# Performance work log

Hardware: AMD Instinct MI355X
Metric: run time of the kernel (lower is better)

Reference implementation:

```python
import jax, jax.numpy as jnp
import numpy as np

N, E_RAW, F_IN, H, C = 50000, 800000, 500, 5, 32
HID = H * C  # 160
NEG_GAT = 0.2   # GATConv leaky_relu slope for attention logits
NEG = 0.01      # F.leaky_relu default slope
LN_EPS = 1e-5


def glorot(key, shape):
    fan_in, fan_out = shape[0], shape[-1]
    lim = jnp.sqrt(6.0 / (fan_in + fan_out))
    return jax.random.uniform(key, shape, jnp.float32, -lim, lim)


def setup_inputs() -> dict:
    key = jax.random.key(0)
    ks = jax.random.split(key, 12)
    x = jax.random.normal(ks[0], (N, F_IN), jnp.float32)
    edge_index = jax.random.randint(ks[1], (2, E_RAW), 0, N, jnp.int64)
    return {
        "x": x,
        "edge_index": edge_index,
        "W1": glorot(ks[2], (F_IN, HID)),
        "att1_s": glorot(ks[3], (H, C)),
        "att1_d": glorot(ks[4], (H, C)),
        "b1": jnp.zeros((HID,), jnp.float32),
        "g1": jnp.ones((HID,), jnp.float32),
        "be1": jnp.zeros((HID,), jnp.float32),
        "W2": glorot(ks[5], (HID, HID)),
        "att2_s": glorot(ks[6], (H, C)),
        "att2_d": glorot(ks[7], (H, C)),
        "b2": jnp.zeros((HID,), jnp.float32),
        "Wm": glorot(ks[8], (HID, HID)),
        "bm": jnp.zeros((HID,), jnp.float32),
    }


def add_self_loops(edge_index):
    loops = jnp.arange(N, dtype=edge_index.dtype)
    return jnp.concatenate([edge_index, jnp.stack([loops, loops])], axis=1)


def gat_conv(x, src, dst, W, att_s, att_d, bias):
    # x: [N, Fin] -> per-head transform [N, H, C]
    xl = (x @ W).reshape(N, H, C)
    a_s = jnp.einsum('nhc,hc->nh', xl, att_s)  # [N, H]
    a_d = jnp.einsum('nhc,hc->nh', xl, att_d)
    logits = jax.nn.leaky_relu(a_s[src] + a_d[dst], NEG_GAT)  # [E, H]
    # segment softmax over incoming edges of each dst node
    lmax = jax.ops.segment_max(logits, dst, num_segments=N)
    alpha = jnp.exp(logits - lmax[dst])
    denom = jax.ops.segment_sum(alpha, dst, num_segments=N)
    alpha = alpha / (denom[dst] + 1e-16)
    msg = xl[src] * alpha[:, :, None]  # [E, H, C]
    out = jax.ops.segment_sum(msg, dst, num_segments=N)
    return out.reshape(N, HID) + bias, alpha


def layer_norm(x, g, b):
    mu = jnp.mean(x, axis=-1, keepdims=True)
    var = jnp.mean((x - mu) ** 2, axis=-1, keepdims=True)
    return (x - mu) * jax.lax.rsqrt(var + LN_EPS) * g + b


def reference(x, edge_index, W1, att1_s, att1_d, b1, g1, be1,
              W2, att2_s, att2_d, b2, Wm, bm):
    ei = add_self_loops(edge_index)
    src, dst = ei[0], ei[1]
    h, alpha1 = gat_conv(x, src, dst, W1, att1_s, att1_d, b1)
    h = jax.nn.leaky_relu(h, NEG)
    h = layer_norm(h, g1, be1)  # dropout is identity in eval mode
    h, alpha2 = gat_conv(h, src, dst, W2, att2_s, att2_d, b2)
    h = jax.nn.leaky_relu(h, NEG)
    out = jax.nn.leaky_relu(h @ Wm + bm, NEG)
    return out, alpha1, alpha2
```

## Files before the change

kernel.cpp:

```cpp
#include <hip/hip_runtime.h>

#define N_NODES 50000
#define E_RAW_N 800000
#define E_TOT   850000
#define F_IN_K  500
#define HID     160
#define XSTR    192

using short8 = __attribute__((ext_vector_type(8))) short;
using f32x4  = __attribute__((ext_vector_type(4))) float;

__device__ __forceinline__ float b2f(unsigned short u) {
  union { unsigned int i; float f; } v; v.i = ((unsigned int)u) << 16; return v.f;
}
__device__ __forceinline__ unsigned short f2b(float f) {
  union { float f; unsigned int i; } v; v.f = f;
  unsigned int i = v.i;
  unsigned int lsb = (i >> 16) & 1u;
  i += 0x7fffu + lsb;
  return (unsigned short)(i >> 16);
}

__device__ __forceinline__ float wsum(float x) {
  #pragma unroll
  for (int o = 32; o; o >>= 1) x += __shfl_xor(x, o, 64);
  return x;
}
__device__ __forceinline__ float wmax(float x) {
  #pragma unroll
  for (int o = 32; o; o >>= 1) x = fmaxf(x, __shfl_xor(x, o, 64));
  return x;
}
__device__ __forceinline__ float lrelu2(float x) { return x > 0.f ? x : 0.2f * x; }

__global__ void detect_kernel(const int* __restrict__ ei, int* __restrict__ flag) {
  if (threadIdx.x == 0 && blockIdx.x == 0) {
    int allz = 1;
    for (int i = 1; i < 128; i += 2) if (ei[i] != 0) { allz = 0; break; }
    *flag = allz;
  }
}
__device__ __forceinline__ int edge_src(const int* ei, int wide, int e) {
  return wide ? ei[2 * e] : ei[e];
}
__device__ __forceinline__ int edge_dst(const int* ei, int wide, int e) {
  return wide ? ei[2 * (E_RAW_N + e)] : ei[E_RAW_N + e];
}

__global__ __launch_bounds__(256) void convert_all(
    const float* __restrict__ W1, const float* __restrict__ W2, const float* __restrict__ Wm,
    unsigned short* __restrict__ Bt1, unsigned short* __restrict__ Bt2,
    unsigned short* __restrict__ Btm)
{
  const int i = blockIdx.x * 256 + threadIdx.x;
  if (i < HID * 512) {
    const int c = i / 512, k = i % 512;
    Bt1[i] = f2b((k < F_IN_K) ? W1[(long)k * HID + c] : 0.f);
  }
  if (i < HID * 192) {
    const int c = i / 192, k = i % 192;
    Bt2[i] = f2b((k < HID) ? W2[(long)k * HID + c] : 0.f);
    Btm[i] = f2b((k < HID) ? Wm[(long)k * HID + c] : 0.f);
  }
}

template<typename AT, int K, int KPAD, int BK, int MODE>
__global__ __launch_bounds__(128) void gemm_lds(
    const AT* __restrict__ A, const unsigned short* __restrict__ Bt,
    float* __restrict__ C, unsigned short* __restrict__ Ch,
    const float* __restrict__ bias,
    const float* __restrict__ att_s, const float* __restrict__ att_d,
    float* __restrict__ a_d)
{
  constexpr bool AB16 = (sizeof(AT) == 2);
  constexpr int LSTR = BK + 8;
  constexpr int CHUNKS = KPAD / BK;
  constexpr int KSC = BK / 32;
  constexpr int ROWU = BK / 8;
  constexpr int UNITS = HID * ROWU;
  static_assert(UNITS % 128 == 0, "units must tile threads");
  constexpr int UPT = UNITS / 128;
  __shared__ __align__(16) unsigned short Bs[HID][LSTR];

  const int t = threadIdx.x;
  const int l = t & 63;
  const int w = t >> 6;
  const int m = l & 15;
  const int kgrp = (l >> 4) * 8;
  const int rbase = blockIdx.x * 32 + w * 16;
  const int arow = (rbase + m < N_NODES) ? rbase + m : N_NODES - 1;
  const AT* Arow = A + (long)arow * K;

  f32x4 acc[10];
  #pragma unroll
  for (int i = 0; i < 10; ++i) acc[i] = (f32x4){0.f, 0.f, 0.f, 0.f};

  short8 rb[UPT];
  float  arF[KSC][8], arF2[KSC][8];
  short8 arS[KSC], arS2[KSC];

  auto loadB = [&](int cc, short8* dst) {
    #pragma unroll
    for (int i = 0; i < UPT; ++i) {
      const int u = i * 128 + t;
      const int c = u / ROWU;
      const int k8 = u % ROWU;
      dst[i] = *(const short8*)(Bt + (long)c * KPAD + cc * BK + k8 * 8);
    }
  };
  auto loadA = [&](int cc, float aF[KSC][8], short8* aS) {
    #pragma unroll
    for (int ks = 0; ks < KSC; ++ks) {
      const int kb = cc * BK + ks * 32 + kgrp;
      if constexpr (AB16) {
        short8 v = (short8){0,0,0,0,0,0,0,0};
        if (kb + 8 <= K) v = *(const short8*)(Arow + kb);
        else if (kb < K) {
          #pragma unroll
          for (int j = 0; j < 8; ++j) v[j] = (kb + j < K) ? (short)Arow[kb + j] : (short)0;
        }
        aS[ks] = v;
      } else {
        if (kb + 8 <= K) {
          const float4 a0 = *(const float4*)(Arow + kb);
          const float4 a1 = *(const float4*)(Arow + kb + 4);
          aF[ks][0]=a0.x; aF[ks][1]=a0.y; aF[ks][2]=a0.z; aF[ks][3]=a0.w;
          aF[ks][4]=a1.x; aF[ks][5]=a1.y; aF[ks][6]=a1.z; aF[ks][7]=a1.w;
        } else {
          #pragma unroll
          for (int j = 0; j < 8; ++j) aF[ks][j] = (kb + j < K) ? (float)Arow[kb + j] : 0.f;
        }
      }
    }
  };

  loadB(0, rb);
  loadA(0, arF, arS);

  for (int cc = 0; cc < CHUNKS; ++cc) {
    __syncthreads();
    #pragma unroll
    for (int i = 0; i < UPT; ++i) {
      const int u = i * 128 + t;
      const int c = u / ROWU;
      const int k8 = u % ROWU;
      *(short8*)&Bs[c][k8 * 8] = rb[i];
    }
    __syncthreads();
    if (cc + 1 < CHUNKS) {
      loadB(cc + 1, rb);
      loadA(cc + 1, arF2, arS2);
      __builtin_amdgcn_sched_barrier(0);
    }
    __builtin_amdgcn_s_setprio(1);
    #pragma unroll
    for (int ks = 0; ks < KSC; ++ks) {
      short8 ah;
      if constexpr (AB16) {
        ah = arS[ks];
      } else {
        #pragma unroll
        for (int j = 0; j < 8; ++j) ah[j] = (short)f2b(arF[ks][j]);
      }
      #pragma unroll
      for (int ct = 0; ct < 10; ++ct) {
        const short8 bh = *(const short8*)&Bs[ct * 16 + m][ks * 32 + kgrp];
        acc[ct] = __builtin_amdgcn_mfma_f32_16x16x32_bf16(ah, bh, acc[ct], 0, 0, 0);
      }
    }
    __builtin_amdgcn_s_setprio(0);
    if (cc + 1 < CHUNKS) {
      #pragma unroll
      for (int ks = 0; ks < KSC; ++ks) {
        if constexpr (AB16) arS[ks] = arS2[ks];
        else {
          #pragma unroll
          for (int j = 0; j < 8; ++j) arF[ks][j] = arF2[ks][j];
        }
      }
    }
  }

  const int crow0 = rbase + (l >> 4) * 4;

  if (MODE == 2) {
    #pragma unroll
    for (int r = 0; r < 4; ++r) {
      float ps[5], pd[5];
      #pragma unroll
      for (int h = 0; h < 5; ++h) {
        float s = acc[2*h][r]     * att_s[(2*h) * 16 + m]
                + acc[2*h + 1][r] * att_s[(2*h + 1) * 16 + m];
        float d = acc[2*h][r]     * att_d[(2*h) * 16 + m]
                + acc[2*h + 1][r] * att_d[(2*h + 1) * 16 + m];
        #pragma unroll
        for (int o = 1; o < 16; o <<= 1) {
          s += __shfl_xor(s, o, 64);
          d += __shfl_xor(d, o, 64);
        }
        ps[h] = s; pd[h] = d;
      }
      const int crow = crow0 + r;
      if (crow < N_NODES && m < 5) {
        const float vs = m == 0 ? ps[0] : m == 1 ? ps[1] : m == 2 ? ps[2] : m == 3 ? ps[3] : ps[4];
        const float vd = m == 0 ? pd[0] : m == 1 ? pd[1] : m == 2 ? pd[2] : m == 3 ? pd[3] : pd[4];
        ((float*)(Ch + (long)crow * XSTR + 160))[m] = vs;
        a_d[crow * 5 + m] = vd;
      }
    }
  }

  #pragma unroll
  for (int r = 0; r < 4; ++r) {
    const int crow = crow0 + r;
    if (crow < N_NODES) {
      #pragma unroll
      for (int ct = 0; ct < 10; ++ct) {
        const int col = ct * 16 + m;
        float v = acc[ct][r];
        if (MODE == 1) { v += bias[col]; v = v > 0.f ? v : 0.01f * v; }
        if (MODE == 2) Ch[(long)crow * XSTR + col] = f2b(v);
        else           C[(long)crow * HID + col] = v;
      }
    }
  }
}

__global__ __launch_bounds__(256) void count_kernel(const int* __restrict__ ei,
    const int* __restrict__ flag, int* __restrict__ deg) {
  const int e = blockIdx.x * 256 + threadIdx.x;
  if (e >= E_TOT) return;
  const int wide = *flag;
  const int d = (e < E_RAW_N) ? edge_dst(ei, wide, e) : (e - E_RAW_N);
  atomicAdd(&deg[d], 1);
}

#define SCAN_CHUNK 49
__global__ __launch_bounds__(1024) void scan_kernel(const int* __restrict__ deg, int* __restrict__ off) {
  __shared__ int wtot[16];
  const int t = threadIdx.x;
  const int lane = t & 63, wid = t >> 6;
  const int base = t * SCAN_CHUNK;
  int local[SCAN_CHUNK];
  int sum = 0;
  #pragma unroll
  for (int i = 0; i < SCAN_CHUNK; ++i) {
    const int idx = base + i;
    const int v = (idx < N_NODES) ? deg[idx] : 0;
    local[i] = sum;
    sum += v;
  }
  int inc = sum;
  #pragma unroll
  for (int o = 1; o < 64; o <<= 1) {
    const int y = __shfl_up(inc, o, 64);
    if (lane >= o) inc += y;
  }
  if (lane == 63) wtot[wid] = inc;
  __syncthreads();
  if (wid == 0 && lane < 16) {
    const int v = wtot[lane];
    int inc2 = v;
    #pragma unroll
    for (int o = 1; o < 16; o <<= 1) {
      const int y = __shfl_up(inc2, o, 64);
      if (lane >= o) inc2 += y;
    }
    wtot[lane] = inc2 - v;
  }
  __syncthreads();
  const int pre = wtot[wid] + (inc - sum);
  #pragma unroll
  for (int i = 0; i < SCAN_CHUNK; ++i) {
    const int idx = base + i;
    if (idx < N_NODES) off[idx] = pre + local[i];
  }
  if (t == 1023) off[N_NODES] = E_TOT;
}

__global__ __launch_bounds__(256) void fill_kernel(const int* __restrict__ ei,
    const int* __restrict__ flag, const int* __restrict__ off,
    int* __restrict__ fillc, int* __restrict__ csr_src, int* __restrict__ csr_eid) {
  const int e = blockIdx.x * 256 + threadIdx.x;
  if (e >= E_TOT) return;
  const int wide = *flag;
  int s, d;
  if (e < E_RAW_N) { s = edge_src(ei, wide, e); d = edge_dst(ei, wide, e); }
  else { s = e - E_RAW_N; d = s; }
  const int p = off[d] + atomicAdd(&fillc[d], 1);
  csr_src[p] = s;
  csr_eid[p] = e;
}

template<int DO_LN>
__global__ __launch_bounds__(256) void node_kernel(
    const int* __restrict__ off_, const int* __restrict__ csr_src, const int* __restrict__ csr_eid,
    const unsigned short* __restrict__ xlh,
    const float* __restrict__ a_d,
    float* __restrict__ alpha_out,
    const float* __restrict__ bias,
    const float* __restrict__ gamma_, const float* __restrict__ beta_,
    unsigned short* __restrict__ hout)
{
  __shared__ int   srcS[4][64];
  __shared__ float alS[4][64][6];

  const int w = threadIdx.x >> 6;
  const int l = threadIdx.x & 63;
  const int n = blockIdx.x * 4 + w;
  if (n >= N_NODES) return;
  const int off = off_[n];
  const int deg = off_[n + 1] - off;

  const float ad0 = a_d[n*5+0], ad1 = a_d[n*5+1], ad2 = a_d[n*5+2], ad3 = a_d[n*5+3], ad4 = a_d[n*5+4];
  const int hA = l >> 4;
  float accx = 0.f, accy = 0.f, accz = 0.f;

  if (deg <= 64) {
    int src = 0, eid = 0;
    float e0 = 0.f, e1 = 0.f, e2 = 0.f, e3 = 0.f, e4 = 0.f;
    if (l < deg) {
      src = csr_src[off + l];
      eid = csr_eid[off + l];
      const float* ap = (const float*)(xlh + (unsigned)src * XSTR + 160);
      e0 = __expf(lrelu2(ap[0] + ad0));
      e1 = __expf(lrelu2(ap[1] + ad1));
      e2 = __expf(lrelu2(ap[2] + ad2));
      e3 = __expf(lrelu2(ap[3] + ad3));
      e4 = __expf(lrelu2(ap[4] + ad4));
    }
    const float i0 = 1.f / (wsum(e0) + 1e-16f), i1 = 1.f / (wsum(e1) + 1e-16f),
                i2 = 1.f / (wsum(e2) + 1e-16f), i3 = 1.f / (wsum(e3) + 1e-16f),
                i4 = 1.f / (wsum(e4) + 1e-16f);
    const float a0 = e0 * i0, a1 = e1 * i1, a2 = e2 * i2, a3 = e3 * i3, a4 = e4 * i4;
    if (l < deg) {
      float* aw = alpha_out + (long)eid * 5;
      aw[0] = a0; aw[1] = a1; aw[2] = a2; aw[3] = a3; aw[4] = a4;
    }
    srcS[w][l] = src;
    alS[w][l][0] = a0; alS[w][l][1] = a1; alS[w][l][2] = a2;
    alS[w][l][3] = a3; alS[w][l][4] = a4;

    const int degR = (deg + 7) & ~7;
    const unsigned cx = 2 * l, cz = 128 + l;
    for (int s0 = 0; s0 < degR; s0 += 8) {
      int sr[8]; float aA[8], aB[8];
      #pragma unroll
      for (int j = 0; j < 8; ++j) {
        sr[j] = srcS[w][s0 + j];
        aA[j] = alS[w][s0 + j][hA];
        aB[j] = alS[w][s0 + j][4];
      }
      ushort2 u2[8]; unsigned short z[8];
      #pragma unroll
      for (int j = 0; j < 8; ++j) {
        const unsigned xb = (unsigned)sr[j] * XSTR;
        u2[j] = *(const ushort2*)(xlh + xb + cx);
        if (l < 32) z[j] = xlh[xb + cz];
      }
      #pragma unroll
      for (int j = 0; j < 8; ++j) {
        accx += b2f(u2[j].x) * aA[j];
        accy += b2f(u2[j].y) * aA[j];
        if (l < 32) accz += b2f(z[j]) * aB[j];
      }
    }
  } else {
    float m0 = -1e30f, m1 = -1e30f, m2 = -1e30f, m3 = -1e30f, m4 = -1e30f;
    for (int s = l; s < deg; s += 64) {
      const float* ap = (const float*)(xlh + (unsigned)csr_src[off + s] * XSTR + 160);
      m0 = fmaxf(m0, lrelu2(ap[0] + ad0));
      m1 = fmaxf(m1, lrelu2(ap[1] + ad1));
      m2 = fmaxf(m2, lrelu2(ap[2] + ad2));
      m3 = fmaxf(m3, lrelu2(ap[3] + ad3));
      m4 = fmaxf(m4, lrelu2(ap[4] + ad4));
    }
    m0 = wmax(m0); m1 = wmax(m1); m2 = wmax(m2); m3 = wmax(m3); m4 = wmax(m4);
    float s0 = 0.f, s1 = 0.f, s2 = 0.f, s3 = 0.f, s4 = 0.f;
    for (int s = l; s < deg; s += 64) {
      const float* ap = (const float*)(xlh + (unsigned)csr_src[off + s] * XSTR + 160);
      s0 += __expf(lrelu2(ap[0] + ad0) - m0);
      s1 += __expf(lrelu2(ap[1] + ad1) - m1);
      s2 += __expf(lrelu2(ap[2] + ad2) - m2);
      s3 += __expf(lrelu2(ap[3] + ad3) - m3);
      s4 += __expf(lrelu2(ap[4] + ad4) - m4);
    }
    const float i0 = 1.f / (wsum(s0) + 1e-16f), i1 = 1.f / (wsum(s1) + 1e-16f),
                i2 = 1.f / (wsum(s2) + 1e-16f), i3 = 1.f / (wsum(s3) + 1e-16f),
                i4 = 1.f / (wsum(s4) + 1e-16f);
    const float adA = hA == 0 ? ad0 : hA == 1 ? ad1 : hA == 2 ? ad2 : ad3;
    const float mA  = hA == 0 ? m0  : hA == 1 ? m1  : hA == 2 ? m2  : m3;
    const float iA  = hA == 0 ? i0  : hA == 1 ? i1  : hA == 2 ? i2  : i3;
    float adw = 0.f, mw = 0.f, iw = 0.f;
    if (l < 5) {
      adw = l == 0 ? ad0 : l == 1 ? ad1 : l == 2 ? ad2 : l == 3 ? ad3 : ad4;
      mw  = l == 0 ? m0  : l == 1 ? m1  : l == 2 ? m2  : l == 3 ? m3  : m4;
      iw  = l == 0 ? i0  : l == 1 ? i1  : l == 2 ? i2  : l == 3 ? i3  : i4;
    }
    for (int s = 0; s < deg; ++s) {
      const int p = off + s;
      const int srcs = csr_src[p];
      const unsigned xb = (unsigned)srcs * XSTR;
      const float* ap = (const float*)(xlh + xb + 160);
      const float aA = __expf(lrelu2(ap[hA] + adA) - mA) * iA;
      const ushort2 u2 = *(const ushort2*)(xlh + xb + 2 * l);
      accx += b2f(u2.x) * aA;
      accy += b2f(u2.y) * aA;
      if (l < 32) {
        const float aC = __expf(lrelu2(ap[4] + ad4) - m4) * i4;
        accz += b2f(xlh[xb + 128 + l]) * aC;
      }
      if (l < 5) {
        alpha_out[(long)csr_eid[p] * 5 + l] = __expf(lrelu2(ap[l] + adw) - mw) * iw;
      }
    }
  }

  const int c0 = 2 * l, c2 = 128 + l;
  float v0 = accx + bias[c0];     v0 = v0 > 0.f ? v0 : 0.01f * v0;
  float v1 = accy + bias[c0 + 1]; v1 = v1 > 0.f ? v1 : 0.01f * v1;
  float v2 = 0.f;
  if (l < 32) { v2 = accz + bias[c2]; v2 = v2 > 0.f ? v2 : 0.01f * v2; }

  const long hb = (long)n * HID;
  if (DO_LN) {
    const float tot = wsum(v0 + v1 + v2);
    const float mean = tot * (1.f / 160.f);
    const float d0 = v0 - mean, d1 = v1 - mean;
    float sq = d0 * d0 + d1 * d1;
    float d2 = 0.f;
    if (l < 32) { d2 = v2 - mean; sq += d2 * d2; }
    const float var = wsum(sq) * (1.f / 160.f);
    const float rstd = rsqrtf(var + 1e-5f);
    hout[hb + c0]     = f2b(d0 * rstd * gamma_[c0]     + beta_[c0]);
    hout[hb + c0 + 1] = f2b(d1 * rstd * gamma_[c0 + 1] + beta_[c0 + 1]);
    if (l < 32) hout[hb + c2] = f2b(d2 * rstd * gamma_[c2] + beta_[c2]);
  } else {
    hout[hb + c0]     = f2b(v0);
    hout[hb + c0 + 1] = f2b(v1);
    if (l < 32) hout[hb + c2] = f2b(v2);
  }
}

extern "C" void kernel_launch(void* const* d_in, const int* in_sizes, int n_in,
                              void* d_out, int out_size, void* d_ws, size_t ws_size,
                              hipStream_t stream)
{
  const float* x     = (const float*)d_in[0];
  const int*   ei    = (const int*)d_in[1];
  const float* W1    = (const float*)d_in[2];
  const float* att1s = (const float*)d_in[3];
  const float* att1d = (const float*)d_in[4];
  const float* b1    = (const float*)d_in[5];
  const float* g1    = (const float*)d_in[6];
  const float* be1   = (const float*)d_in[7];
  const float* W2    = (const float*)d_in[8];
  const float* att2s = (const float*)d_in[9];
  const float* att2d = (const float*)d_in[10];
  const float* b2    = (const float*)d_in[11];
  const float* Wm    = (const float*)d_in[12];
  const float* bm    = (const float*)d_in[13];

  float* out    = (float*)d_out;
  float* alpha1 = out + (long)N_NODES * HID;
  float* alpha2 = alpha1 + (long)E_TOT * 5;

  char* p = (char*)d_ws;
  auto alloc = [&](size_t bytes) { void* r = (void*)p; p += (bytes + 255) & ~(size_t)255; return r; };
  unsigned short* hb16 = (unsigned short*)alloc((size_t)N_NODES * HID * 2);
  unsigned short* xlh  = (unsigned short*)alloc((size_t)N_NODES * XSTR * 2);
  float* ad_  = (float*)alloc((size_t)N_NODES * 5 * 4);
  int* deg    = (int*)alloc((size_t)N_NODES * 4);
  int* fillc  = (int*)alloc((size_t)N_NODES * 4);
  int* off    = (int*)alloc((size_t)(N_NODES + 1) * 4);
  int* csrS   = (int*)alloc((size_t)E_TOT * 4);
  int* csrE   = (int*)alloc((size_t)E_TOT * 4);
  int* flag   = (int*)alloc(256);
  unsigned short* Bt1 = (unsigned short*)alloc((size_t)HID * 512 * 2);
  unsigned short* Bt2 = (unsigned short*)alloc((size_t)HID * 192 * 2);
  unsigned short* Btm = (unsigned short*)alloc((size_t)HID * 192 * 2);

  hipMemsetAsync(deg, 0, (size_t)N_NODES * 4, stream);
  hipMemsetAsync(fillc, 0, (size_t)N_NODES * 4, stream);

  detect_kernel<<<1, 64, 0, stream>>>(ei, flag);
  const int EB = (E_TOT + 255) / 256;
  count_kernel<<<EB, 256, 0, stream>>>(ei, flag, deg);
  scan_kernel<<<1, 1024, 0, stream>>>(deg, off);
  fill_kernel<<<EB, 256, 0, stream>>>(ei, flag, off, fillc, csrS, csrE);

  convert_all<<<(HID * 512 + 255) / 256, 256, 0, stream>>>(W1, W2, Wm, Bt1, Bt2, Btm);

  const int GB = (N_NODES + 31) / 32;

  gemm_lds<float, F_IN_K, 512, 64, 2><<<GB, 128, 0, stream>>>(x, Bt1, nullptr, xlh, nullptr, att1s, att1d, ad_);
  node_kernel<1><<<N_NODES / 4, 256, 0, stream>>>(off, csrS, csrE, xlh, ad_, alpha1, b1, g1, be1, hb16);

  gemm_lds<unsigned short, HID, 192, 64, 2><<<GB, 128, 0, stream>>>(hb16, Bt2, nullptr, xlh, nullptr, att2s, att2d, ad_);
  node_kernel<0><<<N_NODES / 4, 256, 0, stream>>>(off, csrS, csrE, xlh, ad_, alpha2, b2, nullptr, nullptr, hb16);

  gemm_lds<unsigned short, HID, 192, 64, 1><<<GB, 128, 0, stream>>>(hb16, Btm, out, nullptr, bm, nullptr, nullptr, nullptr);
}
```

Before: 399.5 us.

## Stream GEMM B tiles directly into swizzled double-buffered LDS via global_load_lds

Pre-swizzles the bf16 weight matrices into 32-wide K chunks with an XOR pattern. The GEMM now copies each chunk straight from global memory into one of two LDS buffers using global_load_lds, so B no longer passes through registers. This also removes one barrier per chunk and shrinks the K step from 64 to 32, which lowers register pressure but doubles the number of loop iterations. The two degree/fill memsets are merged into one contiguous memset.

```diff
diff --git a/kernel.cpp b/kernel.cpp
--- a/kernel.cpp
+++ b/kernel.cpp
@@ -6,6 +6,7 @@
 #define F_IN_K  500
 #define HID     160
 #define XSTR    192
+#define CHELEMS (HID * 32)
 
 using short8 = __attribute__((ext_vector_type(8))) short;
 using f32x4  = __attribute__((ext_vector_type(4))) float;
@@ -32,6 +33,16 @@
   return x;
 }
 __device__ __forceinline__ float lrelu2(float x) { return x > 0.f ? x : 0.2f * x; }
+
+__device__ __forceinline__ void gload16(const unsigned short* g, unsigned short* l) {
+  __builtin_amdgcn_global_load_lds(
+      (const __attribute__((address_space(1))) void*)g,
+      (__attribute__((address_space(3))) void*)l, 16, 0, 0);
+}
+
+__device__ __forceinline__ int bswz(int c, int kk) {
+  return ((c << 5) | kk) ^ ((c & 7) << 3);
+}
 
 __global__ void detect_kernel(const int* __restrict__ ei, int* __restrict__ flag) {
   if (threadIdx.x == 0 && blockIdx.x == 0) {
@@ -55,16 +66,18 @@
   const int i = blockIdx.x * 256 + threadIdx.x;
   if (i < HID * 512) {
     const int c = i / 512, k = i % 512;
-    Bt1[i] = f2b((k < F_IN_K) ? W1[(long)k * HID + c] : 0.f);
+    const int idx = (k >> 5) * CHELEMS + bswz(c, k & 31);
+    Bt1[idx] = f2b((k < F_IN_K) ? W1[(long)k * HID + c] : 0.f);
   }
   if (i < HID * 192) {
     const int c = i / 192, k = i % 192;
-    Bt2[i] = f2b((k < HID) ? W2[(long)k * HID + c] : 0.f);
-    Btm[i] = f2b((k < HID) ? Wm[(long)k * HID + c] : 0.f);
-  }
-}
-
-template<typename AT, int K, int KPAD, int BK, int MODE>
+    const int idx = (k >> 5) * CHELEMS + bswz(c, k & 31);
+    Bt2[idx] = f2b((k < HID) ? W2[(long)k * HID + c] : 0.f);
+    Btm[idx] = f2b((k < HID) ? Wm[(long)k * HID + c] : 0.f);
+  }
+}
+
+template<typename AT, int K, int KPAD, int MODE>
 __global__ __launch_bounds__(128) void gemm_lds(
     const AT* __restrict__ A, const unsigned short* __restrict__ Bt,
     float* __restrict__ C, unsigned short* __restrict__ Ch,
@@ -73,14 +86,8 @@
     float* __restrict__ a_d)
 {
   constexpr bool AB16 = (sizeof(AT) == 2);
-  constexpr int LSTR = BK + 8;
-  constexpr int CHUNKS = KPAD / BK;
-  constexpr int KSC = BK / 32;
-  constexpr int ROWU = BK / 8;
-  constexpr int UNITS = HID * ROWU;
-  static_assert(UNITS % 128 == 0, "units must tile threads");
-  constexpr int UPT = UNITS / 128;
-  __shared__ __align__(16) unsigned short Bs[HID][LSTR];
+  constexpr int CHUNKS = KPAD / 32;
+  __shared__ __align__(16) unsigned short Bs[2][CHELEMS];
 
   const int t = threadIdx.x;
   const int l = t & 63;
@@ -95,88 +102,71 @@
   #pragma unroll
   for (int i = 0; i < 10; ++i) acc[i] = (f32x4){0.f, 0.f, 0.f, 0.f};
 
-  short8 rb[UPT];
-  float  arF[KSC][8], arF2[KSC][8];
-  short8 arS[KSC], arS2[KSC];
-
-  auto loadB = [&](int cc, short8* dst) {
+  float  arF[8], arF2[8];
+  short8 arS, arS2;
+
+  auto issueB = [&](int cc) {
+    const unsigned short* src = Bt + (long)cc * CHELEMS;
+    unsigned short* dst = &Bs[cc & 1][0];
     #pragma unroll
-    for (int i = 0; i < UPT; ++i) {
-      const int u = i * 128 + t;
-      const int c = u / ROWU;
-      const int k8 = u % ROWU;
-      dst[i] = *(const short8*)(Bt + (long)c * KPAD + cc * BK + k8 * 8);
+    for (int j = 0; j < 5; ++j) {
+      const int base = (j * 2 + w) * 512;
+      gload16(src + base + l * 8, dst + base);
     }
   };
-  auto loadA = [&](int cc, float aF[KSC][8], short8* aS) {
-    #pragma unroll
-    for (int ks = 0; ks < KSC; ++ks) {
-      const int kb = cc * BK + ks * 32 + kgrp;
-      if constexpr (AB16) {
-        short8 v = (short8){0,0,0,0,0,0,0,0};
-        if (kb + 8 <= K) v = *(const short8*)(Arow + kb);
-        else if (kb < K) {
-          #pragma unroll
-          for (int j = 0; j < 8; ++j) v[j] = (kb + j < K) ? (short)Arow[kb + j] : (short)0;
-        }
-        aS[ks] = v;
+  auto loadA = [&](int cc, float* aF, short8& aS) {
+    const int kb = cc * 32 + kgrp;
+    if constexpr (AB16) {
+      short8 v = (short8){0,0,0,0,0,0,0,0};
+      if (kb + 8 <= K) v = *(const short8*)(Arow + kb);
+      else if (kb < K) {
+        #pragma unroll
+        for (int j = 0; j < 8; ++j) v[j] = (kb + j < K) ? (short)Arow[kb + j] : (short)0;
+      }
+      aS = v;
+    } else {
+      if (kb + 8 <= K) {
+        const float4 a0 = *(const float4*)(Arow + kb);
+        const float4 a1 = *(const float4*)(Arow + kb + 4);
+        aF[0]=a0.x; aF[1]=a0.y; aF[2]=a0.z; aF[3]=a0.w;
+        aF[4]=a1.x; aF[5]=a1.y; aF[6]=a1.z; aF[7]=a1.w;
       } else {
-        if (kb + 8 <= K) {
-          const float4 a0 = *(const float4*)(Arow + kb);
-          const float4 a1 = *(const float4*)(Arow + kb + 4);
-          aF[ks][0]=a0.x; aF[ks][1]=a0.y; aF[ks][2]=a0.z; aF[ks][3]=a0.w;
-          aF[ks][4]=a1.x; aF[ks][5]=a1.y; aF[ks][6]=a1.z; aF[ks][7]=a1.w;
-        } else {
-          #pragma unroll
-          for (int j = 0; j < 8; ++j) aF[ks][j] = (kb + j < K) ? (float)Arow[kb + j] : 0.f;
-        }
+        #pragma unroll
+        for (int j = 0; j < 8; ++j) aF[j] = (kb + j < K) ? (float)Arow[kb + j] : 0.f;
       }
     }
   };
 
-  loadB(0, rb);
+  issueB(0);
   loadA(0, arF, arS);
 
   for (int cc = 0; cc < CHUNKS; ++cc) {
     __syncthreads();
-    #pragma unroll
-    for (int i = 0; i < UPT; ++i) {
-      const int u = i * 128 + t;
-      const int c = u / ROWU;
-      const int k8 = u % ROWU;
-      *(short8*)&Bs[c][k8 * 8] = rb[i];
-    }
-    __syncthreads();
     if (cc + 1 < CHUNKS) {
-      loadB(cc + 1, rb);
+      issueB(cc + 1);
       loadA(cc + 1, arF2, arS2);
       __builtin_amdgcn_sched_barrier(0);
     }
     __builtin_amdgcn_s_setprio(1);
+    short8 ah;
+    if constexpr (AB16) {
+      ah = arS;
+    } else {
+      #pragma unroll
+      for (int j = 0; j < 8; ++j) ah[j] = (short)f2b(arF[j]);
+    }
     #pragma unroll
-    for (int ks = 0; ks < KSC; ++ks) {
-      short8 ah;
-      if constexpr (AB16) {
-        ah = arS[ks];
-      } else {
-        #pragma unroll
-        for (int j = 0; j < 8; ++j) ah[j] = (short)f2b(arF[ks][j]);
-      }
-      #pragma unroll
-      for (int ct = 0; ct < 10; ++ct) {
-        const short8 bh = *(const short8*)&Bs[ct * 16 + m][ks * 32 + kgrp];
-        acc[ct] = __builtin_amdgcn_mfma_f32_16x16x32_bf16(ah, bh, acc[ct], 0, 0, 0);
-      }
+    for (int ct = 0; ct < 10; ++ct) {
+      const int c = ct * 16 + m;
+      const short8 bh = *(const short8*)&Bs[cc & 1][bswz(c, kgrp)];
+      acc[ct] = __builtin_amdgcn_mfma_f32_16x16x32_bf16(ah, bh, acc[ct], 0, 0, 0);
     }
     __builtin_amdgcn_s_setprio(0);
     if (cc + 1 < CHUNKS) {
-      #pragma unroll
-      for (int ks = 0; ks < KSC; ++ks) {
-        if constexpr (AB16) arS[ks] = arS2[ks];
-        else {
-          #pragma unroll
-          for (int j = 0; j < 8; ++j) arF[ks][j] = arF2[ks][j];
-        }
+      if constexpr (AB16) arS = arS2;
+      else {
+        #pragma unroll
+        for (int j = 0; j < 8; ++j) arF[j] = arF2[j];
       }
     }
   }
@@ -480,8 +470,7 @@
   unsigned short* Bt2 = (unsigned short*)alloc((size_t)HID * 192 * 2);
   unsigned short* Btm = (unsigned short*)alloc((size_t)HID * 192 * 2);
 
-  hipMemsetAsync(deg, 0, (size_t)N_NODES * 4, stream);
-  hipMemsetAsync(fillc, 0, (size_t)N_NODES * 4, stream);
+  hipMemsetAsync(deg, 0, (size_t)((char*)off - (char*)deg), stream);
 
   detect_kernel<<<1, 64, 0, stream>>>(ei, flag);
   const int EB = (E_TOT + 255) / 256;
@@ -493,11 +482,11 @@
 
   const int GB = (N_NODES + 31) / 32;
 
-  gemm_lds<float, F_IN_K, 512, 64, 2><<<GB, 128, 0, stream>>>(x, Bt1, nullptr, xlh, nullptr, att1s, att1d, ad_);
+  gemm_lds<float, F_IN_K, 512, 2><<<GB, 128, 0, stream>>>(x, Bt1, nullptr, xlh, nullptr, att1s, att1d, ad_);
   node_kernel<1><<<N_NODES / 4, 256, 0, stream>>>(off, csrS, csrE, xlh, ad_, alpha1, b1, g1, be1, hb16);
 
-  gemm_lds<unsigned short, HID, 192, 64, 2><<<GB, 128, 0, stream>>>(hb16, Bt2, nullptr, xlh, nullptr, att2s, att2d, ad_);
+  gemm_lds<unsigned short, HID, 192, 2><<<GB, 128, 0, stream>>>(hb16, Bt2, nullptr, xlh, nullptr, att2s, att2d, ad_);
   node_kernel<0><<<N_NODES / 4, 256, 0, stream>>>(off, csrS, csrE, xlh, ad_, alpha2, b2, nullptr, nullptr, hb16);
 
-  gemm_lds<unsigned short, HID, 192, 64, 1><<<GB, 128, 0, stream>>>(hb16, Btm, out, nullptr, bm, nullptr, nullptr, nullptr);
-}
+  gemm_lds<unsigned short, HID, 192, 1><<<GB, 128, 0, stream>>>(hb16, Btm, out, nullptr, bm, nullptr, nullptr, nullptr);
+}
```

After: 396.6 us. No clear change (-0.7%).
